# Kernel optimization log

Hardware: AMD Instinct MI355X
Metric: run time of the kernel (lower is better)

## Reference

```python
import jax, jax.numpy as jnp
import numpy as np

B, S, D, H = 2, 2048, 1024, 16
HD = D // H  # 64
SCALE = HD ** -0.5


def setup_inputs() -> dict:
    key = jax.random.key(0)
    ks = jax.random.split(key, 11)
    std = D ** -0.5
    inp = {
        "q": jax.random.normal(ks[0], (B, S, D), jnp.float32),
        "k": jax.random.normal(ks[1], (B, S, D), jnp.float32),
        "v": jax.random.normal(ks[2], (B, S, D), jnp.float32),
        # causal mask: True = masked (strictly upper triangular)
        "attn_mask": jnp.triu(jnp.ones((S, S), jnp.bool_), k=1),
        "Wq": jax.random.normal(ks[3], (D, D), jnp.float32) * std,
        "bq": jnp.zeros((D,), jnp.float32),
        "Wk": jax.random.normal(ks[4], (D, D), jnp.float32) * std,
        "bk": jnp.zeros((D,), jnp.float32),
        "Wv": jax.random.normal(ks[5], (D, D), jnp.float32) * std,
        "bv": jnp.zeros((D,), jnp.float32),
        "Wo": jax.random.normal(ks[6], (D, D), jnp.float32) * std,
        "bo": jnp.zeros((D,), jnp.float32),
    }
    return inp


def reference(q, k, v, attn_mask, Wq, bq, Wk, bk, Wv, bv, Wo, bo):
    # projections (torch Linear: x @ W.T + b), split into heads: [B,H,S,HD]
    def heads(x, W, b):
        y = jnp.einsum("bsd,ed->bse", x, W) + b
        return y.reshape(B, S, H, HD).transpose(0, 2, 1, 3)

    qh = heads(q, Wq, bq)
    kh = heads(k, Wk, bk)
    vh = heads(v, Wv, bv)

    # scaled dot-product attention with mask (True = blocked)
    scores = jnp.einsum("bhqd,bhkd->bhqk", qh, kh) * SCALE
    scores = jnp.where(attn_mask[None, None, :, :], -jnp.inf, scores)
    weights = jax.nn.softmax(scores, axis=-1)
    out = jnp.einsum("bhqk,bhkd->bhqd", weights, vh)

    # merge heads and output projection
    out = out.transpose(0, 2, 1, 3).reshape(B, S, D)
    return jnp.einsum("bsd,ed->bse", out, Wo) + bo
```

## Files before the change

### kernel.cpp

```cpp
#include <hip/hip_runtime.h>
#include <hip/hip_bf16.h>

typedef __attribute__((ext_vector_type(8))) short bf16x8;
typedef __attribute__((ext_vector_type(4))) float f32x4;

#define NB 2
#define NS 2048
#define ND 1024
#define NH 16
#define NHD 64
#define ATTN_SCALE 0.125f

__device__ __forceinline__ unsigned short f2bf(float f) {
    union { float f; unsigned int u; } x; x.f = f;
    unsigned int r = x.u + 0x7fffu + ((x.u >> 16) & 1u);
    return (unsigned short)(r >> 16);
}

__device__ __forceinline__ void gload16(const void* g, void* l) {
    __builtin_amdgcn_global_load_lds(
        (const __attribute__((address_space(1))) unsigned int*)g,
        (__attribute__((address_space(3))) unsigned int*)l, 16, 0, 0);
}

__device__ __forceinline__ void cvt_store16(unsigned short* p,
        const float4& a0, const float4& a1, const float4& a2, const float4& a3) {
    uint4 u0, u1;
    u0.x = (unsigned)f2bf(a0.x) | ((unsigned)f2bf(a0.y) << 16);
    u0.y = (unsigned)f2bf(a0.z) | ((unsigned)f2bf(a0.w) << 16);
    u0.z = (unsigned)f2bf(a1.x) | ((unsigned)f2bf(a1.y) << 16);
    u0.w = (unsigned)f2bf(a1.z) | ((unsigned)f2bf(a1.w) << 16);
    u1.x = (unsigned)f2bf(a2.x) | ((unsigned)f2bf(a2.y) << 16);
    u1.y = (unsigned)f2bf(a2.z) | ((unsigned)f2bf(a2.w) << 16);
    u1.z = (unsigned)f2bf(a3.x) | ((unsigned)f2bf(a3.y) << 16);
    u1.w = (unsigned)f2bf(a3.z) | ((unsigned)f2bf(a3.w) << 16);
    ((uint4*)p)[0] = u0;
    ((uint4*)p)[1] = u1;
}

__global__ __launch_bounds__(256) void cvt_kernel(
    const float* __restrict__ s0, const float* __restrict__ s1,
    const float* __restrict__ s2, const float* __restrict__ s3,
    unsigned short* __restrict__ d0, unsigned short* __restrict__ d1,
    unsigned short* __restrict__ d2, unsigned short* __restrict__ d3, int n)
{
    const float* s = (blockIdx.y == 0) ? s0 : (blockIdx.y == 1) ? s1 : (blockIdx.y == 2) ? s2 : s3;
    unsigned short* d = (blockIdx.y == 0) ? d0 : (blockIdx.y == 1) ? d1 : (blockIdx.y == 2) ? d2 : d3;
    const int i = (blockIdx.x * 256 + threadIdx.x) * 8;
    if (i >= n) return;
    const float4* sp = (const float4*)(s + i);
    const float4 a = sp[0], b = sp[1];
    uint4 u;
    u.x = (unsigned)f2bf(a.x) | ((unsigned)f2bf(a.y) << 16);
    u.y = (unsigned)f2bf(a.z) | ((unsigned)f2bf(a.w) << 16);
    u.z = (unsigned)f2bf(b.x) | ((unsigned)f2bf(b.y) << 16);
    u.w = (unsigned)f2bf(b.z) | ((unsigned)f2bf(b.w) << 16);
    *(uint4*)(d + i) = u;
}

__global__ __launch_bounds__(256) void qkv2_kernel(
    const unsigned short* __restrict__ xq, const unsigned short* __restrict__ xk,
    const unsigned short* __restrict__ xv,
    const unsigned short* __restrict__ wq, const unsigned short* __restrict__ wk,
    const unsigned short* __restrict__ wv,
    const float* __restrict__ bq, const float* __restrict__ bk, const float* __restrict__ bv,
    unsigned short* __restrict__ qh, unsigned short* __restrict__ kh, unsigned short* __restrict__ vt)
{
    __shared__ __align__(16) unsigned short lds[2][2][128 * 32];
    const int t = threadIdx.x;
    const int lane = t & 63;
    const int wid = t >> 6;
    const int wm = wid >> 1, wn = wid & 1;
    const int lq = lane & 15, g = lane >> 4;
    const int bm = blockIdx.x;
    const int mat = blockIdx.y >> 3;
    const int bn = blockIdx.y & 7;

    const unsigned short* x = (mat == 0) ? xq : (mat == 1) ? xk : xv;
    const unsigned short* W = (mat == 0) ? wq : (mat == 1) ? wk : wv;
    const float* bias = (mat == 0) ? bq : (mat == 1) ? bk : bv;
    unsigned short* dst = (mat == 0) ? qh : (mat == 1) ? kh : vt;
    const float scale = (mat == 0) ? ATTN_SCALE : 1.0f;

    const char* abyte = (const char*)x;
    const char* bbyte = (const char*)W;
    const int rowl0 = (2 * wid + 0) * 16 + (lane >> 2);
    const int rowl1 = (2 * wid + 1) * 16 + (lane >> 2);
    const int colb = (lane & 3) * 16;
    const size_t abase0 = (size_t)(bm * 128 + rowl0) * 2048 + colb;
    const size_t abase1 = (size_t)(bm * 128 + rowl1) * 2048 + colb;
    const size_t bbase0 = (size_t)(bn * 128 + rowl0) * 2048 + colb;
    const size_t bbase1 = (size_t)(bn * 128 + rowl1) * 2048 + colb;

    f32x4 acc[4][4];
    const f32x4 zero = {0.f, 0.f, 0.f, 0.f};
#pragma unroll
    for (int m = 0; m < 4; ++m)
#pragma unroll
        for (int n = 0; n < 4; ++n) acc[m][n] = zero;

    auto STAGE = [&](int kt, int bufi) {
        const size_t ko = (size_t)kt * 64;
        gload16(abyte + abase0 + ko, (char*)&lds[bufi][0][0] + (2 * wid + 0) * 1024);
        gload16(abyte + abase1 + ko, (char*)&lds[bufi][0][0] + (2 * wid + 1) * 1024);
        gload16(bbyte + bbase0 + ko, (char*)&lds[bufi][1][0] + (2 * wid + 0) * 1024);
        gload16(bbyte + bbase1 + ko, (char*)&lds[bufi][1][0] + (2 * wid + 1) * 1024);
    };

    STAGE(0, 0);
    asm volatile("s_waitcnt vmcnt(0)" ::: "memory");
    __syncthreads();

    for (int kt = 0; kt < 32; ++kt) {
        const int cur = kt & 1;
        if (kt < 31) STAGE(kt + 1, cur ^ 1);
        bf16x8 af[4], bfr[4];
#pragma unroll
        for (int m = 0; m < 4; ++m)
            af[m] = *(const bf16x8*)&lds[cur][0][(wm * 64 + m * 16 + lq) * 32 + g * 8];
#pragma unroll
        for (int n = 0; n < 4; ++n)
            bfr[n] = *(const bf16x8*)&lds[cur][1][(wn * 64 + n * 16 + lq) * 32 + g * 8];
#pragma unroll
        for (int m = 0; m < 4; ++m)
#pragma unroll
            for (int n = 0; n < 4; ++n)
                acc[m][n] = __builtin_amdgcn_mfma_f32_16x16x32_bf16(af[m], bfr[n], acc[m][n], 0, 0, 0);
        __syncthreads();
    }

    const int row0 = bm * 128 + wm * 64;
    const int col0 = bn * 128 + wn * 64;
#pragma unroll
    for (int n = 0; n < 4; ++n) {
        const int col = col0 + n * 16 + lq;
        const float bb = bias[col];
        const int h = col >> 6, hd = col & 63;
#pragma unroll
        for (int m = 0; m < 4; ++m) {
#pragma unroll
            for (int r = 0; r < 4; ++r) {
                const int row = row0 + m * 16 + g * 4 + r;
                const int b = row >> 11, s = row & (NS - 1);
                const float v = (acc[m][n][r] + bb) * scale;
                size_t o;
                if (mat == 2) o = ((size_t)((b * NH + h) * NHD + hd)) * NS + s;
                else          o = ((size_t)((b * NH + h) * NS + s)) * NHD + hd;
                dst[o] = f2bf(v);
            }
        }
    }
}

__global__ __launch_bounds__(256, 2) void attn3_kernel(
    const unsigned short* __restrict__ qh, const unsigned short* __restrict__ kh,
    const unsigned short* __restrict__ vt, unsigned short* __restrict__ ao)
{
    __shared__ __align__(16) unsigned short plds[4][32 * 72];
    const int t = threadIdx.x, lane = t & 63, wid = t >> 6;
    const int lq = lane & 15, g = lane >> 4;

    const int i = blockIdx.x;
    int bh, qblk;
    if (i < 256) { bh = i & 31; qblk = 15 - (i >> 5); }
    else { const int j = i - 256; bh = j & 31; qblk = j >> 5; }
    const int b = bh >> 4, h = bh & 15;

    const unsigned short* qb = qh + (size_t)bh * NS * NHD;
    const unsigned short* kb = kh + (size_t)bh * NS * NHD;
    const unsigned short* vb = vt + (size_t)bh * NS * NHD;
    unsigned short* pw = plds[wid];
    const int q0w = qblk * 128 + wid * 32;

    bf16x8 qf[2][2];
#pragma unroll
    for (int qs = 0; qs < 2; ++qs)
#pragma unroll
        for (int ks = 0; ks < 2; ++ks)
            qf[qs][ks] = *(const bf16x8*)&qb[(size_t)(q0w + qs * 16 + lq) * NHD + ks * 32 + g * 8];

    f32x4 accO[4][2];
    const f32x4 zero = {0.f, 0.f, 0.f, 0.f};
#pragma unroll
    for (int c = 0; c < 4; ++c) { accO[c][0] = zero; accO[c][1] = zero; }
    float mrun[2] = {-INFINITY, -INFINITY};
    float lsum[2] = {0.f, 0.f};

    auto LOADK = [&](bf16x8 (&kf)[2][4], int tile) {
        const int kv0 = tile * 64;
#pragma unroll
        for (int ks = 0; ks < 2; ++ks)
#pragma unroll
            for (int kv = 0; kv < 4; ++kv)
                kf[ks][kv] = *(const bf16x8*)&kb[(size_t)(kv0 + kv * 16 + lq) * NHD + ks * 32 + g * 8];
    };
    auto LOADV = [&](bf16x8 (&vf)[2][4], int tile) {
        const int kv0 = tile * 64;
#pragma unroll
        for (int ks = 0; ks < 2; ++ks)
#pragma unroll
            for (int c = 0; c < 4; ++c)
                vf[ks][c] = *(const bf16x8*)&vb[(size_t)(c * 16 + lq) * NS + kv0 + ks * 32 + g * 8];
    };

    auto TILE = [&](int tile, bf16x8 (&kf)[2][4], bf16x8 (&vf)[2][4]) {
        const int kv0 = tile * 64;
        f32x4 st[4][2];
#pragma unroll
        for (int kv = 0; kv < 4; ++kv) { st[kv][0] = zero; st[kv][1] = zero; }
#pragma unroll
        for (int ks = 0; ks < 2; ++ks)
#pragma unroll
            for (int kv = 0; kv < 4; ++kv) {
                st[kv][0] = __builtin_amdgcn_mfma_f32_16x16x32_bf16(kf[ks][kv], qf[0][ks], st[kv][0], 0, 0, 0);
                st[kv][1] = __builtin_amdgcn_mfma_f32_16x16x32_bf16(kf[ks][kv], qf[1][ks], st[kv][1], 0, 0, 0);
            }
        if (kv0 + 63 > q0w) {
#pragma unroll
            for (int kv = 0; kv < 4; ++kv)
#pragma unroll
                for (int r = 0; r < 4; ++r) {
                    const int kvi = kv0 + kv * 16 + g * 4 + r;
#pragma unroll
                    for (int qs = 0; qs < 2; ++qs) {
                        const int qi = q0w + qs * 16 + lq;
                        if (kvi > qi) st[kv][qs][r] = -1e30f;
                    }
                }
        }
#pragma unroll
        for (int qs = 0; qs < 2; ++qs) {
            float tmax = st[0][qs][0];
#pragma unroll
            for (int kv = 0; kv < 4; ++kv)
#pragma unroll
                for (int r = 0; r < 4; ++r) tmax = fmaxf(tmax, st[kv][qs][r]);
            tmax = fmaxf(tmax, __shfl_xor(tmax, 16));
            tmax = fmaxf(tmax, __shfl_xor(tmax, 32));
            const float mnew = fmaxf(mrun[qs], tmax);
            const float alpha = __expf(mrun[qs] - mnew);
            float ls = 0.f;
#pragma unroll
            for (int kv = 0; kv < 4; ++kv)
#pragma unroll
                for (int r = 0; r < 4; ++r) {
                    const float p = __expf(st[kv][qs][r] - mnew);
                    st[kv][qs][r] = p;
                    ls += p;
                }
            ls += __shfl_xor(ls, 16);
            ls += __shfl_xor(ls, 32);
            lsum[qs] = lsum[qs] * alpha + ls;
            mrun[qs] = mnew;
#pragma unroll
            for (int c = 0; c < 4; ++c) accO[c][qs] *= alpha;
#pragma unroll
            for (int kv = 0; kv < 4; ++kv) {
                const unsigned u0 = (unsigned)f2bf(st[kv][qs][0]) | ((unsigned)f2bf(st[kv][qs][1]) << 16);
                const unsigned u1 = (unsigned)f2bf(st[kv][qs][2]) | ((unsigned)f2bf(st[kv][qs][3]) << 16);
                unsigned short* base = &pw[(qs * 16 + lq) * 72 + kv * 16 + g * 4];
                *(unsigned*)base = u0;
                *(unsigned*)(base + 2) = u1;
            }
        }
        asm volatile("s_waitcnt lgkmcnt(0)" ::: "memory");
#pragma unroll
        for (int ks = 0; ks < 2; ++ks) {
            const bf16x8 pb0 = *(const bf16x8*)&pw[(0 + lq) * 72 + ks * 32 + g * 8];
            const bf16x8 pb1 = *(const bf16x8*)&pw[(16 + lq) * 72 + ks * 32 + g * 8];
#pragma unroll
            for (int c = 0; c < 4; ++c) {
                accO[c][0] = __builtin_amdgcn_mfma_f32_16x16x32_bf16(vf[ks][c], pb0, accO[c][0], 0, 0, 0);
                accO[c][1] = __builtin_amdgcn_mfma_f32_16x16x32_bf16(vf[ks][c], pb1, accO[c][1], 0, 0, 0);
            }
        }
    };

    const int Tw = ((q0w + 31) >> 6) + 1;
    bf16x8 kfA[2][4], kfB[2][4], vf[2][4];
    LOADK(kfA, 0);
    int tt = 0;
    for (; tt + 1 < Tw; tt += 2) {
        LOADV(vf, tt);
        LOADK(kfB, tt + 1);
        TILE(tt, kfA, vf);
        LOADV(vf, tt + 1);
        if (tt + 2 < Tw) LOADK(kfA, tt + 2);
        TILE(tt + 1, kfB, vf);
    }
    if (tt < Tw) {
        LOADV(vf, tt);
        TILE(tt, kfA, vf);
    }

#pragma unroll
    for (int qs = 0; qs < 2; ++qs) {
        const float inv = 1.0f / lsum[qs];
        const int q = q0w + qs * 16 + lq;
        unsigned short* aobase = ao + ((size_t)b * NS + q) * ND + h * NHD;
#pragma unroll
        for (int c = 0; c < 4; ++c) {
            uint2 w2;
            w2.x = (unsigned)f2bf(accO[c][qs][0] * inv) | ((unsigned)f2bf(accO[c][qs][1] * inv) << 16);
            w2.y = (unsigned)f2bf(accO[c][qs][2] * inv) | ((unsigned)f2bf(accO[c][qs][3] * inv) << 16);
            *(uint2*)&aobase[c * 16 + g * 4] = w2;
        }
    }
}

__global__ __launch_bounds__(256) void oproj2_kernel(
    const unsigned short* __restrict__ ao, const unsigned short* __restrict__ wo,
    const float* __restrict__ bo, float* __restrict__ out)
{
    __shared__ __align__(16) unsigned short lds[2][2][128 * 32];
    const int t = threadIdx.x;
    const int lane = t & 63;
    const int wid = t >> 6;
    const int wm = wid >> 1, wn = wid & 1;
    const int lq = lane & 15, g = lane >> 4;
    const int bm = blockIdx.x;
    const int bn = blockIdx.y;

    const char* abyte = (const char*)ao;
    const char* bbyte = (const char*)wo;
    const int rowl0 = (2 * wid + 0) * 16 + (lane >> 2);
    const int rowl1 = (2 * wid + 1) * 16 + (lane >> 2);
    const int colb = (lane & 3) * 16;
    const size_t abase0 = (size_t)(bm * 128 + rowl0) * 2048 + colb;
    const size_t abase1 = (size_t)(bm * 128 + rowl1) * 2048 + colb;
    const size_t bbase0 = (size_t)(bn * 128 + rowl0) * 2048 + colb;
    const size_t bbase1 = (size_t)(bn * 128 + rowl1) * 2048 + colb;

    f32x4 acc[4][4];
    const f32x4 zero = {0.f, 0.f, 0.f, 0.f};
#pragma unroll
    for (int m = 0; m < 4; ++m)
#pragma unroll
        for (int n = 0; n < 4; ++n) acc[m][n] = zero;

    auto STAGE = [&](int kt, int bufi) {
        const size_t ko = (size_t)kt * 64;
        gload16(abyte + abase0 + ko, (char*)&lds[bufi][0][0] + (2 * wid + 0) * 1024);
        gload16(abyte + abase1 + ko, (char*)&lds[bufi][0][0] + (2 * wid + 1) * 1024);
        gload16(bbyte + bbase0 + ko, (char*)&lds[bufi][1][0] + (2 * wid + 0) * 1024);
        gload16(bbyte + bbase1 + ko, (char*)&lds[bufi][1][0] + (2 * wid + 1) * 1024);
    };

    STAGE(0, 0);
    asm volatile("s_waitcnt vmcnt(0)" ::: "memory");
    __syncthreads();

    for (int kt = 0; kt < 32; ++kt) {
        const int cur = kt & 1;
        if (kt < 31) STAGE(kt + 1, cur ^ 1);
        bf16x8 af[4], bfr[4];
#pragma unroll
        for (int m = 0; m < 4; ++m)
            af[m] = *(const bf16x8*)&lds[cur][0][(wm * 64 + m * 16 + lq) * 32 + g * 8];
#pragma unroll
        for (int n = 0; n < 4; ++n)
            bfr[n] = *(const bf16x8*)&lds[cur][1][(wn * 64 + n * 16 + lq) * 32 + g * 8];
#pragma unroll
        for (int m = 0; m < 4; ++m)
#pragma unroll
            for (int n = 0; n < 4; ++n)
                acc[m][n] = __builtin_amdgcn_mfma_f32_16x16x32_bf16(af[m], bfr[n], acc[m][n], 0, 0, 0);
        __syncthreads();
    }

    const int row0 = bm * 128 + wm * 64;
    const int col0 = bn * 128 + wn * 64;
#pragma unroll
    for (int n = 0; n < 4; ++n) {
        const int col = col0 + n * 16 + lq;
        const float bb = bo[col];
#pragma unroll
        for (int m = 0; m < 4; ++m) {
#pragma unroll
            for (int r = 0; r < 4; ++r) {
                const int row = row0 + m * 16 + g * 4 + r;
                out[(size_t)row * ND + col] = acc[m][n][r] + bb;
            }
        }
    }
}

__global__ __launch_bounds__(256) void qkv_proj_kernel(
    const float* __restrict__ xq, const float* __restrict__ xk, const float* __restrict__ xv,
    const float* __restrict__ Wq, const float* __restrict__ Wk, const float* __restrict__ Wv,
    const float* __restrict__ bq, const float* __restrict__ bk, const float* __restrict__ bv,
    unsigned short* __restrict__ qh, unsigned short* __restrict__ kh, unsigned short* __restrict__ vt)
{
    __shared__ __align__(16) unsigned short lds[2][2][128 * 32];
    const int t = threadIdx.x;
    const int lane = t & 63;
    const int wid = t >> 6;
    const int wm = wid >> 1, wn = wid & 1;
    const int lq = lane & 15, g = lane >> 4;
    const int bm = blockIdx.x;
    const int mat = blockIdx.y >> 3;
    const int bn = blockIdx.y & 7;

    const float* x = (mat == 0) ? xq : (mat == 1) ? xk : xv;
    const float* W = (mat == 0) ? Wq : (mat == 1) ? Wk : Wv;
    const float* bias = (mat == 0) ? bq : (mat == 1) ? bk : bv;
    unsigned short* dst = (mat == 0) ? qh : (mat == 1) ? kh : vt;
    const float scale = (mat == 0) ? ATTN_SCALE : 1.0f;

    const int srow = t >> 1;
    const int scol = (t & 1) << 4;
    const float* aptr = x + (size_t)(bm * 128 + srow) * ND + scol;
    const float* bptr = W + (size_t)(bn * 128 + srow) * ND + scol;
    const int soff = srow * 32 + scol;

    f32x4 acc[4][4];
    const f32x4 zero = {0.f, 0.f, 0.f, 0.f};
#pragma unroll
    for (int m = 0; m < 4; ++m)
#pragma unroll
        for (int n = 0; n < 4; ++n) acc[m][n] = zero;

    {
        const float4* ap = (const float4*)aptr;
        float4 A0 = ap[0], A1 = ap[1], A2 = ap[2], A3 = ap[3];
        const float4* bp = (const float4*)bptr;
        float4 B0 = bp[0], B1 = bp[1], B2 = bp[2], B3 = bp[3];
        cvt_store16(&lds[0][0][soff], A0, A1, A2, A3);
        cvt_store16(&lds[0][1][soff], B0, B1, B2, B3);
    }
    __syncthreads();

    for (int kt = 0; kt < ND / 32; ++kt) {
        const int cur = kt & 1;
        float4 A0, A1, A2, A3, B0, B1, B2, B3;
        if (kt < ND / 32 - 1) {
            const float4* ap = (const float4*)(aptr + (kt + 1) * 32);
            A0 = ap[0]; A1 = ap[1]; A2 = ap[2]; A3 = ap[3];
            const float4* bp = (const float4*)(bptr + (kt + 1) * 32);
            B0 = bp[0]; B1 = bp[1]; B2 = bp[2]; B3 = bp[3];
        }
        bf16x8 af[4], bfr[4];
#pragma unroll
        for (int m = 0; m < 4; ++m)
            af[m] = *(const bf16x8*)&lds[cur][0][(wm * 64 + m * 16 + lq) * 32 + g * 8];
#pragma unroll
        for (int n = 0; n < 4; ++n)
            bfr[n] = *(const bf16x8*)&lds[cur][1][(wn * 64 + n * 16 + lq) * 32 + g * 8];
#pragma unroll
        for (int m = 0; m < 4; ++m)
#pragma unroll
            for (int n = 0; n < 4; ++n)
                acc[m][n] = __builtin_amdgcn_mfma_f32_16x16x32_bf16(af[m], bfr[n], acc[m][n], 0, 0, 0);
        if (kt < ND / 32 - 1) {
            cvt_store16(&lds[cur ^ 1][0][soff], A0, A1, A2, A3);
            cvt_store16(&lds[cur ^ 1][1][soff], B0, B1, B2, B3);
        }
        __syncthreads();
    }

    const int row0 = bm * 128 + wm * 64;
    const int col0 = bn * 128 + wn * 64;
#pragma unroll
    for (int n = 0; n < 4; ++n) {
        const int col = col0 + n * 16 + lq;
        const float bb = bias[col];
        const int h = col >> 6, hd = col & 63;
#pragma unroll
        for (int m = 0; m < 4; ++m) {
#pragma unroll
            for (int r = 0; r < 4; ++r) {
                const int row = row0 + m * 16 + g * 4 + r;
                const int b = row >> 11, s = row & (NS - 1);
                const float v = (acc[m][n][r] + bb) * scale;
                size_t o;
                if (mat == 2) o = ((size_t)((b * NH + h) * NHD + hd)) * NS + s;
                else          o = ((size_t)((b * NH + h) * NS + s)) * NHD + hd;
                dst[o] = f2bf(v);
            }
        }
    }
}

__global__ __launch_bounds__(256) void out_proj_kernel(
    const unsigned short* __restrict__ ao, const float* __restrict__ Wo,
    const float* __restrict__ bo, float* __restrict__ out)
{
    __shared__ __align__(16) unsigned short lds[2][2][128 * 32];
    const int t = threadIdx.x;
    const int lane = t & 63;
    const int wid = t >> 6;
    const int wm = wid >> 1, wn = wid & 1;
    const int lq = lane & 15, g = lane >> 4;
    const int bm = blockIdx.x;
    const int bn = blockIdx.y;

    const int srow = t >> 1;
    const int scol = (t & 1) << 4;
    const unsigned short* aptr = ao + (size_t)(bm * 128 + srow) * ND + scol;
    const float* bptr = Wo + (size_t)(bn * 128 + srow) * ND + scol;
    const int soff = srow * 32 + scol;

    f32x4 acc[4][4];
    const f32x4 zero = {0.f, 0.f, 0.f, 0.f};
#pragma unroll
    for (int m = 0; m < 4; ++m)
#pragma unroll
        for (int n = 0; n < 4; ++n) acc[m][n] = zero;

    {
        const uint4* ap = (const uint4*)aptr;
        uint4 V0 = ap[0], V1 = ap[1];
        const float4* bp = (const float4*)bptr;
        float4 B0 = bp[0], B1 = bp[1], B2 = bp[2], B3 = bp[3];
        ((uint4*)&lds[0][0][soff])[0] = V0;
        ((uint4*)&lds[0][0][soff])[1] = V1;
        cvt_store16(&lds[0][1][soff], B0, B1, B2, B3);
    }
    __syncthreads();

    for (int kt = 0; kt < ND / 32; ++kt) {
        const int cur = kt & 1;
        uint4 V0, V1;
        float4 B0, B1, B2, B3;
        if (kt < ND / 32 - 1) {
            const uint4* ap = (const uint4*)(aptr + (kt + 1) * 32);
            V0 = ap[0]; V1 = ap[1];
            const float4* bp = (const float4*)(bptr + (kt + 1) * 32);
            B0 = bp[0]; B1 = bp[1]; B2 = bp[2]; B3 = bp[3];
        }
        bf16x8 af[4], bfr[4];
#pragma unroll
        for (int m = 0; m < 4; ++m)
            af[m] = *(const bf16x8*)&lds[cur][0][(wm * 64 + m * 16 + lq) * 32 + g * 8];
#pragma unroll
        for (int n = 0; n < 4; ++n)
            bfr[n] = *(const bf16x8*)&lds[cur][1][(wn * 64 + n * 16 + lq) * 32 + g * 8];
#pragma unroll
        for (int m = 0; m < 4; ++m)
#pragma unroll
            for (int n = 0; n < 4; ++n)
                acc[m][n] = __builtin_amdgcn_mfma_f32_16x16x32_bf16(af[m], bfr[n], acc[m][n], 0, 0, 0);
        if (kt < ND / 32 - 1) {
            ((uint4*)&lds[cur ^ 1][0][soff])[0] = V0;
            ((uint4*)&lds[cur ^ 1][0][soff])[1] = V1;
            cvt_store16(&lds[cur ^ 1][1][soff], B0, B1, B2, B3);
        }
        __syncthreads();
    }

    const int row0 = bm * 128 + wm * 64;
    const int col0 = bn * 128 + wn * 64;
#pragma unroll
    for (int n = 0; n < 4; ++n) {
        const int col = col0 + n * 16 + lq;
        const float bb = bo[col];
#pragma unroll
        for (int m = 0; m < 4; ++m) {
#pragma unroll
            for (int r = 0; r < 4; ++r) {
                const int row = row0 + m * 16 + g * 4 + r;
                out[(size_t)row * ND + col] = acc[m][n][r] + bb;
            }
        }
    }
}

extern "C" void kernel_launch(void* const* d_in, const int* in_sizes, int n_in,
                              void* d_out, int out_size, void* d_ws, size_t ws_size,
                              hipStream_t stream) {
    const float* q  = (const float*)d_in[0];
    const float* k  = (const float*)d_in[1];
    const float* v  = (const float*)d_in[2];
    const float* Wq = (const float*)d_in[4];
    const float* bq = (const float*)d_in[5];
    const float* Wk = (const float*)d_in[6];
    const float* bk = (const float*)d_in[7];
    const float* Wv = (const float*)d_in[8];
    const float* bv = (const float*)d_in[9];
    const float* Wo = (const float*)d_in[10];
    const float* bo = (const float*)d_in[11];

    const size_t elems = (size_t)NB * NS * ND;
    const size_t welems = (size_t)ND * ND;
    unsigned short* qh  = (unsigned short*)d_ws;
    unsigned short* kh  = qh + elems;
    unsigned short* vt  = kh + elems;
    unsigned short* ao  = vt + elems;
    unsigned short* xqb = ao + elems;
    unsigned short* xkb = xqb + elems;
    unsigned short* xvb = xkb + elems;
    unsigned short* wqb = xvb + elems;
    unsigned short* wkb = wqb + welems;
    unsigned short* wvb = wkb + welems;
    unsigned short* wob = wvb + welems;
    const size_t need = (size_t)(4 + 3) * elems * 2 + (size_t)4 * welems * 2;

    if (ws_size >= need) {
        cvt_kernel<<<dim3(2048, 3), 256, 0, stream>>>(q, k, v, q, xqb, xkb, xvb, xqb, (int)elems);
        cvt_kernel<<<dim3(512, 4), 256, 0, stream>>>(Wq, Wk, Wv, Wo, wqb, wkb, wvb, wob, (int)welems);
        qkv2_kernel<<<dim3(32, 24), 256, 0, stream>>>(xqb, xkb, xvb, wqb, wkb, wvb, bq, bk, bv, qh, kh, vt);
        attn3_kernel<<<dim3(512), 256, 0, stream>>>(qh, kh, vt, ao);
        oproj2_kernel<<<dim3(32, 8), 256, 0, stream>>>(ao, wob, bo, (float*)d_out);
    } else {
        qkv_proj_kernel<<<dim3(32, 24), 256, 0, stream>>>(q, k, v, Wq, Wk, Wv, bq, bk, bv, qh, kh, vt);
        attn3_kernel<<<dim3(512), 256, 0, stream>>>(qh, kh, vt, ao);
        out_proj_kernel<<<dim3(32, 8), 256, 0, stream>>>(ao, Wo, bo, (float*)d_out);
    }
}
```

Before: 258.5 us.

## Rewrite attention with 32x32 MFMA and register-only P via permlane32 swap

The attention kernel switches from 16x16x32 to 32x32x16 bf16 MFMAs, with each wave handling 32 query rows in a single accumulator layout. The softmax probabilities are packed with v_cvt_pk_bf16_f32 and rearranged between half-waves with permlane32_swap, which removes the LDS round-trip and waitcnt for P. It also adds a lazy rescale that skips the alpha update unless the running max grows by more than 8, and simplifies K prefetch to a single buffer. The cost is less explicit K/V double-buffering and a new dependence on gfx950-specific instructions.

```diff
diff --git a/kernel.cpp b/kernel.cpp
--- a/kernel.cpp
+++ b/kernel.cpp
@@ -3,6 +3,7 @@
 
 typedef __attribute__((ext_vector_type(8))) short bf16x8;
 typedef __attribute__((ext_vector_type(4))) float f32x4;
+typedef __attribute__((ext_vector_type(16))) float f32x16;
 
 #define NB 2
 #define NS 2048
@@ -15,6 +16,12 @@
     union { float f; unsigned int u; } x; x.f = f;
     unsigned int r = x.u + 0x7fffu + ((x.u >> 16) & 1u);
     return (unsigned short)(r >> 16);
+}
+
+__device__ __forceinline__ unsigned cvtpk(float lo, float hi) {
+    unsigned r;
+    asm("v_cvt_pk_bf16_f32 %0, %1, %2" : "=v"(r) : "v"(lo), "v"(hi));
+    return r;
 }
 
 __device__ __forceinline__ void gload16(const void* g, void* l) {
@@ -152,13 +159,12 @@
     }
 }
 
-__global__ __launch_bounds__(256, 2) void attn3_kernel(
+__global__ __launch_bounds__(256, 2) void attn4_kernel(
     const unsigned short* __restrict__ qh, const unsigned short* __restrict__ kh,
     const unsigned short* __restrict__ vt, unsigned short* __restrict__ ao)
 {
-    __shared__ __align__(16) unsigned short plds[4][32 * 72];
     const int t = threadIdx.x, lane = t & 63, wid = t >> 6;
-    const int lq = lane & 15, g = lane >> 4;
+    const int q32 = lane & 31, hi = lane >> 5;
 
     const int i = blockIdx.x;
     int bh, qblk;
@@ -169,143 +175,127 @@
     const unsigned short* qb = qh + (size_t)bh * NS * NHD;
     const unsigned short* kb = kh + (size_t)bh * NS * NHD;
     const unsigned short* vb = vt + (size_t)bh * NS * NHD;
-    unsigned short* pw = plds[wid];
     const int q0w = qblk * 128 + wid * 32;
-
-    bf16x8 qf[2][2];
-#pragma unroll
-    for (int qs = 0; qs < 2; ++qs)
-#pragma unroll
-        for (int ks = 0; ks < 2; ++ks)
-            qf[qs][ks] = *(const bf16x8*)&qb[(size_t)(q0w + qs * 16 + lq) * NHD + ks * 32 + g * 8];
-
-    f32x4 accO[4][2];
-    const f32x4 zero = {0.f, 0.f, 0.f, 0.f};
-#pragma unroll
-    for (int c = 0; c < 4; ++c) { accO[c][0] = zero; accO[c][1] = zero; }
-    float mrun[2] = {-INFINITY, -INFINITY};
-    float lsum[2] = {0.f, 0.f};
-
-    auto LOADK = [&](bf16x8 (&kf)[2][4], int tile) {
+    const int q = q0w + q32;
+
+    bf16x8 qf[4];
+#pragma unroll
+    for (int ks = 0; ks < 4; ++ks)
+        qf[ks] = *(const bf16x8*)&qb[(size_t)q * NHD + ks * 16 + hi * 8];
+
+    f32x16 accO[2];
+#pragma unroll
+    for (int r = 0; r < 16; ++r) { accO[0][r] = 0.f; accO[1][r] = 0.f; }
+    float mrun = -INFINITY, lsum = 0.f;
+
+    const int Tw = ((q0w + 31) >> 6) + 1;
+
+    bf16x8 kf[2][4];
+#pragma unroll
+    for (int kvb = 0; kvb < 2; ++kvb)
+#pragma unroll
+        for (int ks = 0; ks < 4; ++ks)
+            kf[kvb][ks] = *(const bf16x8*)&kb[(size_t)(kvb * 32 + q32) * NHD + ks * 16 + hi * 8];
+
+    for (int tile = 0; tile < Tw; ++tile) {
         const int kv0 = tile * 64;
-#pragma unroll
-        for (int ks = 0; ks < 2; ++ks)
-#pragma unroll
-            for (int kv = 0; kv < 4; ++kv)
-                kf[ks][kv] = *(const bf16x8*)&kb[(size_t)(kv0 + kv * 16 + lq) * NHD + ks * 32 + g * 8];
-    };
-    auto LOADV = [&](bf16x8 (&vf)[2][4], int tile) {
-        const int kv0 = tile * 64;
-#pragma unroll
-        for (int ks = 0; ks < 2; ++ks)
-#pragma unroll
-            for (int c = 0; c < 4; ++c)
-                vf[ks][c] = *(const bf16x8*)&vb[(size_t)(c * 16 + lq) * NS + kv0 + ks * 32 + g * 8];
-    };
-
-    auto TILE = [&](int tile, bf16x8 (&kf)[2][4], bf16x8 (&vf)[2][4]) {
-        const int kv0 = tile * 64;
-        f32x4 st[4][2];
-#pragma unroll
-        for (int kv = 0; kv < 4; ++kv) { st[kv][0] = zero; st[kv][1] = zero; }
-#pragma unroll
-        for (int ks = 0; ks < 2; ++ks)
-#pragma unroll
-            for (int kv = 0; kv < 4; ++kv) {
-                st[kv][0] = __builtin_amdgcn_mfma_f32_16x16x32_bf16(kf[ks][kv], qf[0][ks], st[kv][0], 0, 0, 0);
-                st[kv][1] = __builtin_amdgcn_mfma_f32_16x16x32_bf16(kf[ks][kv], qf[1][ks], st[kv][1], 0, 0, 0);
+
+        bf16x8 vf[2][4];
+#pragma unroll
+        for (int hb = 0; hb < 2; ++hb)
+#pragma unroll
+            for (int ks = 0; ks < 4; ++ks)
+                vf[hb][ks] = *(const bf16x8*)&vb[(size_t)(hb * 32 + q32) * NS + kv0 + ks * 16 + hi * 8];
+
+        f32x16 st[2];
+#pragma unroll
+        for (int r = 0; r < 16; ++r) { st[0][r] = 0.f; st[1][r] = 0.f; }
+#pragma unroll
+        for (int ks = 0; ks < 4; ++ks) {
+            st[0] = __builtin_amdgcn_mfma_f32_32x32x16_bf16(kf[0][ks], qf[ks], st[0], 0, 0, 0);
+            st[1] = __builtin_amdgcn_mfma_f32_32x32x16_bf16(kf[1][ks], qf[ks], st[1], 0, 0, 0);
+        }
+
+        if (tile + 1 < Tw) {
+            const int nkv0 = kv0 + 64;
+#pragma unroll
+            for (int kvb = 0; kvb < 2; ++kvb)
+#pragma unroll
+                for (int ks = 0; ks < 4; ++ks)
+                    kf[kvb][ks] = *(const bf16x8*)&kb[(size_t)(nkv0 + kvb * 32 + q32) * NHD + ks * 16 + hi * 8];
+        }
+
+        if (kv0 + 63 > q0w) {
+#pragma unroll
+            for (int kvb = 0; kvb < 2; ++kvb)
+#pragma unroll
+                for (int r = 0; r < 16; ++r) {
+                    const int kvi = kv0 + kvb * 32 + (r & 3) + 8 * (r >> 2) + 4 * hi;
+                    if (kvi > q) st[kvb][r] = -1e30f;
+                }
+        }
+
+        float tmax = st[0][0];
+#pragma unroll
+        for (int r = 1; r < 16; ++r) tmax = fmaxf(tmax, st[0][r]);
+#pragma unroll
+        for (int r = 0; r < 16; ++r) tmax = fmaxf(tmax, st[1][r]);
+        tmax = fmaxf(tmax, __shfl_xor(tmax, 32));
+
+        if (!__all(tmax <= mrun + 8.f)) {
+            const float mnew = fmaxf(mrun, tmax);
+            const float alpha = __expf(mrun - mnew);
+            lsum *= alpha;
+#pragma unroll
+            for (int r = 0; r < 16; ++r) { accO[0][r] *= alpha; accO[1][r] *= alpha; }
+            mrun = mnew;
+        }
+        float ls = 0.f;
+#pragma unroll
+        for (int kvb = 0; kvb < 2; ++kvb)
+#pragma unroll
+            for (int r = 0; r < 16; ++r) {
+                const float p = __expf(st[kvb][r] - mrun);
+                st[kvb][r] = p;
+                ls += p;
             }
-        if (kv0 + 63 > q0w) {
-#pragma unroll
-            for (int kv = 0; kv < 4; ++kv)
-#pragma unroll
-                for (int r = 0; r < 4; ++r) {
-                    const int kvi = kv0 + kv * 16 + g * 4 + r;
-#pragma unroll
-                    for (int qs = 0; qs < 2; ++qs) {
-                        const int qi = q0w + qs * 16 + lq;
-                        if (kvi > qi) st[kv][qs][r] = -1e30f;
-                    }
-                }
-        }
-#pragma unroll
-        for (int qs = 0; qs < 2; ++qs) {
-            float tmax = st[0][qs][0];
-#pragma unroll
-            for (int kv = 0; kv < 4; ++kv)
-#pragma unroll
-                for (int r = 0; r < 4; ++r) tmax = fmaxf(tmax, st[kv][qs][r]);
-            tmax = fmaxf(tmax, __shfl_xor(tmax, 16));
-            tmax = fmaxf(tmax, __shfl_xor(tmax, 32));
-            const float mnew = fmaxf(mrun[qs], tmax);
-            const float alpha = __expf(mrun[qs] - mnew);
-            float ls = 0.f;
-#pragma unroll
-            for (int kv = 0; kv < 4; ++kv)
-#pragma unroll
-                for (int r = 0; r < 4; ++r) {
-                    const float p = __expf(st[kv][qs][r] - mnew);
-                    st[kv][qs][r] = p;
-                    ls += p;
-                }
-            ls += __shfl_xor(ls, 16);
-            ls += __shfl_xor(ls, 32);
-            lsum[qs] = lsum[qs] * alpha + ls;
-            mrun[qs] = mnew;
-#pragma unroll
-            for (int c = 0; c < 4; ++c) accO[c][qs] *= alpha;
-#pragma unroll
-            for (int kv = 0; kv < 4; ++kv) {
-                const unsigned u0 = (unsigned)f2bf(st[kv][qs][0]) | ((unsigned)f2bf(st[kv][qs][1]) << 16);
-                const unsigned u1 = (unsigned)f2bf(st[kv][qs][2]) | ((unsigned)f2bf(st[kv][qs][3]) << 16);
-                unsigned short* base = &pw[(qs * 16 + lq) * 72 + kv * 16 + g * 4];
-                *(unsigned*)base = u0;
-                *(unsigned*)(base + 2) = u1;
-            }
-        }
-        asm volatile("s_waitcnt lgkmcnt(0)" ::: "memory");
-#pragma unroll
-        for (int ks = 0; ks < 2; ++ks) {
-            const bf16x8 pb0 = *(const bf16x8*)&pw[(0 + lq) * 72 + ks * 32 + g * 8];
-            const bf16x8 pb1 = *(const bf16x8*)&pw[(16 + lq) * 72 + ks * 32 + g * 8];
-#pragma unroll
-            for (int c = 0; c < 4; ++c) {
-                accO[c][0] = __builtin_amdgcn_mfma_f32_16x16x32_bf16(vf[ks][c], pb0, accO[c][0], 0, 0, 0);
-                accO[c][1] = __builtin_amdgcn_mfma_f32_16x16x32_bf16(vf[ks][c], pb1, accO[c][1], 0, 0, 0);
-            }
-        }
-    };
-
-    const int Tw = ((q0w + 31) >> 6) + 1;
-    bf16x8 kfA[2][4], kfB[2][4], vf[2][4];
-    LOADK(kfA, 0);
-    int tt = 0;
-    for (; tt + 1 < Tw; tt += 2) {
-        LOADV(vf, tt);
-        LOADK(kfB, tt + 1);
-        TILE(tt, kfA, vf);
-        LOADV(vf, tt + 1);
-        if (tt + 2 < Tw) LOADK(kfA, tt + 2);
-        TILE(tt + 1, kfB, vf);
-    }
-    if (tt < Tw) {
-        LOADV(vf, tt);
-        TILE(tt, kfA, vf);
-    }
-
-#pragma unroll
-    for (int qs = 0; qs < 2; ++qs) {
-        const float inv = 1.0f / lsum[qs];
-        const int q = q0w + qs * 16 + lq;
-        unsigned short* aobase = ao + ((size_t)b * NS + q) * ND + h * NHD;
-#pragma unroll
-        for (int c = 0; c < 4; ++c) {
+        ls += __shfl_xor(ls, 32);
+        lsum += ls;
+
+        bf16x8 pb[4];
+#pragma unroll
+        for (int ks = 0; ks < 4; ++ks) {
+            const int kvb = ks >> 1;
+            const int base = (ks & 1) * 8;
+            const unsigned x0 = cvtpk(st[kvb][base + 0], st[kvb][base + 1]);
+            const unsigned y0 = cvtpk(st[kvb][base + 4], st[kvb][base + 5]);
+            const unsigned x1 = cvtpk(st[kvb][base + 2], st[kvb][base + 3]);
+            const unsigned y1 = cvtpk(st[kvb][base + 6], st[kvb][base + 7]);
+            auto r02 = __builtin_amdgcn_permlane32_swap(x0, y0, false, false);
+            auto r13 = __builtin_amdgcn_permlane32_swap(x1, y1, false, false);
+            union { unsigned u[4]; bf16x8 v; } pk;
+            pk.u[0] = r02[0]; pk.u[1] = r13[0]; pk.u[2] = r02[1]; pk.u[3] = r13[1];
+            pb[ks] = pk.v;
+        }
+
+#pragma unroll
+        for (int ks = 0; ks < 4; ++ks) {
+            accO[0] = __builtin_amdgcn_mfma_f32_32x32x16_bf16(vf[0][ks], pb[ks], accO[0], 0, 0, 0);
+            accO[1] = __builtin_amdgcn_mfma_f32_32x32x16_bf16(vf[1][ks], pb[ks], accO[1], 0, 0, 0);
+        }
+    }
+
+    const float inv = 1.0f / lsum;
+    unsigned short* aobase = ao + ((size_t)b * NS + q) * ND + h * NHD;
+#pragma unroll
+    for (int hb = 0; hb < 2; ++hb)
+#pragma unroll
+        for (int rg = 0; rg < 4; ++rg) {
             uint2 w2;
-            w2.x = (unsigned)f2bf(accO[c][qs][0] * inv) | ((unsigned)f2bf(accO[c][qs][1] * inv) << 16);
-            w2.y = (unsigned)f2bf(accO[c][qs][2] * inv) | ((unsigned)f2bf(accO[c][qs][3] * inv) << 16);
-            *(uint2*)&aobase[c * 16 + g * 4] = w2;
-        }
-    }
+            w2.x = cvtpk(accO[hb][4 * rg + 0] * inv, accO[hb][4 * rg + 1] * inv);
+            w2.y = cvtpk(accO[hb][4 * rg + 2] * inv, accO[hb][4 * rg + 3] * inv);
+            *(uint2*)&aobase[hb * 32 + 8 * rg + 4 * hi] = w2;
+        }
 }
 
 __global__ __launch_bounds__(256) void oproj2_kernel(
@@ -599,11 +589,11 @@
         cvt_kernel<<<dim3(2048, 3), 256, 0, stream>>>(q, k, v, q, xqb, xkb, xvb, xqb, (int)elems);
         cvt_kernel<<<dim3(512, 4), 256, 0, stream>>>(Wq, Wk, Wv, Wo, wqb, wkb, wvb, wob, (int)welems);
         qkv2_kernel<<<dim3(32, 24), 256, 0, stream>>>(xqb, xkb, xvb, wqb, wkb, wvb, bq, bk, bv, qh, kh, vt);
-        attn3_kernel<<<dim3(512), 256, 0, stream>>>(qh, kh, vt, ao);
+        attn4_kernel<<<dim3(512), 256, 0, stream>>>(qh, kh, vt, ao);
         oproj2_kernel<<<dim3(32, 8), 256, 0, stream>>>(ao, wob, bo, (float*)d_out);
     } else {
         qkv_proj_kernel<<<dim3(32, 24), 256, 0, stream>>>(q, k, v, Wq, Wk, Wv, bq, bk, bv, qh, kh, vt);
-        attn3_kernel<<<dim3(512), 256, 0, stream>>>(qh, kh, vt, ao);
+        attn4_kernel<<<dim3(512), 256, 0, stream>>>(qh, kh, vt, ao);
         out_proj_kernel<<<dim3(32, 8), 256, 0, stream>>>(ao, Wo, bo, (float*)d_out);
     }
 }
```

Result: no change. 255.3 us (-1.2%).
